# Kernel optimization log

Hardware: AMD Instinct MI355X
Metric: run time of the kernel (lower is better)

## Reference

```python
import jax, jax.numpy as jnp
import numpy as np

HIDDEN = 32
ODE_H = 0.1      # rk4 fixed step size (torchdiffeq options step_size=0.1)
ODE_STEPS = 10   # integrate t in [0, 1]


def gcn_conv(x, W, b, edge_index, n):
    """PyG GCNConv: symmetric norm with self-loops; x' = D^-1/2 (A+I) D^-1/2 (x W) + b."""
    h = x @ W                                  # [n, out]
    src, dst = edge_index[0], edge_index[1]
    deg = jnp.ones((n,), h.dtype).at[dst].add(1.0)   # +1 for self-loop
    dinv = jax.lax.rsqrt(deg)
    coef = (dinv[src] * dinv[dst])[:, None]
    agg = jnp.zeros_like(h).at[dst].add(h[src] * coef)
    agg = agg + h * (dinv * dinv)[:, None]     # self-loop term
    return agg + b


def ode_rk4(x0, edge_index, Wg, bg, wt, n):
    """RK4 integration of psi(t,x)=relu(GCN(x)) * sigmoid(t * wt) from t=0 to 1."""
    def f(t, x):
        gate = jax.nn.sigmoid(t * wt)          # [hidden], Linear(1,h,no bias).sigmoid()
        return jax.nn.relu(gcn_conv(x, Wg, bg, edge_index, n)) * gate

    h = ODE_H
    def step(x, t):
        k1 = f(t, x)
        k2 = f(t + h * 0.5, x + (h * 0.5) * k1)
        k3 = f(t + h * 0.5, x + (h * 0.5) * k2)
        k4 = f(t + h, x + h * k3)
        return x + (h / 6.0) * (k1 + 2.0 * k2 + 2.0 * k3 + k4), None

    ts = jnp.arange(ODE_STEPS, dtype=x0.dtype) * h
    xf, _ = jax.lax.scan(step, x0, ts)
    return xf


def setup_inputs() -> dict:
    key = jax.random.key(0)
    ks = jax.random.split(key, 16)
    N, IN, H = 100000, 128, HIDDEN
    E, DE = 1600000, 800000

    inp = {
        "H_t": jax.random.normal(ks[0], (N, IN), jnp.float32),
        "A_pos_t": jax.random.randint(ks[1], (2, E), 0, N),
        "A_neg_t": jax.random.randint(ks[2], (2, E), 0, N),
        "dA_pos": jax.random.randint(ks[3], (2, DE), 0, N),
        "dA_neg": jax.random.randint(ks[4], (2, DE), 0, N),
        # init GCN
        "W_init": jax.random.normal(ks[5], (IN, H), jnp.float32) / np.sqrt(IN),
        "b_init": jnp.zeros((H,), jnp.float32),
        # pos ODE func
        "W_pos": jax.random.normal(ks[6], (H, H), jnp.float32) / np.sqrt(H),
        "b_pos": jnp.zeros((H,), jnp.float32),
        "wt_pos": jax.random.normal(ks[7], (H,), jnp.float32),
        # neg ODE func
        "W_neg": jax.random.normal(ks[8], (H, H), jnp.float32) / np.sqrt(H),
        "b_neg": jnp.zeros((H,), jnp.float32),
        "wt_neg": jax.random.normal(ks[9], (H,), jnp.float32),
        # combine + layernorm
        "W_comb": jax.random.normal(ks[10], (2 * H, H), jnp.float32) / np.sqrt(2 * H),
        "b_comb": jnp.zeros((H,), jnp.float32),
        "ln_g": jnp.ones((H,), jnp.float32),
        "ln_b": jnp.zeros((H,), jnp.float32),
    }
    return inp


def reference(H_t, A_pos_t, A_neg_t, dA_pos, dA_neg,
              W_init, b_init, W_pos, b_pos, wt_pos,
              W_neg, b_neg, wt_neg, W_comb, b_comb, ln_g, ln_b):
    n = H_t.shape[0]
    edges_all = jnp.concatenate([A_pos_t, A_neg_t], axis=1)
    H = jax.nn.relu(gcn_conv(H_t, W_init, b_init, edges_all, n))   # [n, hidden]
    Z_pos = ode_rk4(H, dA_pos, W_pos, b_pos, wt_pos, n)
    Z_neg = ode_rk4(H, dA_neg, W_neg, b_neg, wt_neg, n)
    Z = jnp.concatenate([Z_pos, Z_neg], axis=-1) @ W_comb + b_comb # [n, hidden]
    mu = jnp.mean(Z, axis=-1, keepdims=True)
    var = jnp.var(Z, axis=-1, keepdims=True)
    return (Z - mu) * jax.lax.rsqrt(var + 1e-5) * ln_g + ln_b
```

## Files before the change

### kernel.cpp

```cpp
#include <hip/hip_runtime.h>
#include <math.h>


#define TPB 256
#define SCAN_T 1024

typedef _Float16 h8 __attribute__((ext_vector_type(8)));
typedef float f8 __attribute__((ext_vector_type(8)));


struct SegG { const int* src; const int* dst; int n; int goff; };
struct FSeg { const int* src; const int* dst; int n; const int* offs; int* cur; };

__global__ __launch_bounds__(TPB) void count_mm(
        SegG s0, SegG s1, SegG s2, SegG s3, int* __restrict__ cnt3,
        unsigned short* __restrict__ rank,
        const float* __restrict__ x, const float* __restrict__ W,
        float* __restrict__ temp, int N, int cntB, int mmB) {
    __shared__ float Ws[128][32];
    __shared__ float xs[8][128];

    int g5 = blockIdx.x / 5, r5 = blockIdx.x % 5;
    if (r5 < 3) {
        int cb = g5 * 3 + r5;
        if (cb >= cntB) return;
        int i = cb * TPB + threadIdx.x;
        SegG s; int e;
        if (i < s0.n) { s = s0; e = i; }
        else if (i < s0.n + s1.n) { s = s1; e = i - s0.n; }
        else if (i < s0.n + s1.n + s2.n) { s = s2; e = i - s0.n - s1.n; }
        else if (i < s0.n + s1.n + s2.n + s3.n) { s = s3; e = i - s0.n - s1.n - s2.n; }
        else return;
        int r = atomicAdd(&cnt3[s.goff + s.dst[e]], 1);
        if (rank) rank[i] = (unsigned short)r;
    } else {
        int mb = g5 * 2 + (r5 - 3);
        if (mb >= mmB) return;
        int tid = threadIdx.x;
        for (int i = tid; i < 128 * 32; i += TPB) Ws[i >> 5][i & 31] = W[i];
        int base = mb * 8;
        for (int i = tid; i < 8 * 128; i += TPB) {
            int idx = base * 128 + i;
            xs[i >> 7][i & 127] = (idx < N * 128) ? x[idx] : 0.0f;
        }
        __syncthreads();
        int row = tid >> 5, c = tid & 31;
        int gr = base + row;
        float acc = 0.0f;
#pragma unroll
        for (int k = 0; k < 128; ++k) acc += xs[row][k] * Ws[k][c];
        if (gr < N) temp[gr * 32 + c] = acc;
    }
}

__global__ __launch_bounds__(TPB) void fill_scale(
        SegG s0, SegG s1, SegG s2, SegG s3,
        const int* __restrict__ offs3, const unsigned short* __restrict__ rank,
        int* __restrict__ csr,
        const float* __restrict__ temp, const float* __restrict__ dinv,
        _Float16* __restrict__ hs, int N, int fillB, int scaleB) {
    int g13 = blockIdx.x / 13, r13 = blockIdx.x % 13;
    if (r13 < 12) {
        int fb = g13 * 12 + r13;
        if (fb >= fillB) return;
        int i = fb * TPB + threadIdx.x;
        SegG s; int e;
        if (i < s0.n) { s = s0; e = i; }
        else if (i < s0.n + s1.n) { s = s1; e = i - s0.n; }
        else if (i < s0.n + s1.n + s2.n) { s = s2; e = i - s0.n - s1.n; }
        else if (i < s0.n + s1.n + s2.n + s3.n) { s = s3; e = i - s0.n - s1.n - s2.n; }
        else return;
        csr[offs3[s.goff + s.dst[e]] + (int)rank[i]] = s.src[e];
    } else {
        int c = g13 * TPB + threadIdx.x;
        if (c < N * 4) {
            f8 v = ((const f8*)temp)[c];
            float dv = dinv[c >> 2];
            ((h8*)hs)[c] = __builtin_convertvector(v * dv, h8);
        }
    }
}

__global__ void scale_hs(const float* __restrict__ temp, const float* __restrict__ dinv,
                         _Float16* __restrict__ hs, int N) {
    int c = blockIdx.x * blockDim.x + threadIdx.x;
    if (c < N * 4) {
        f8 v = ((const f8*)temp)[c];
        ((h8*)hs)[c] = __builtin_convertvector(v * dinv[c >> 2], h8);
    }
}

__global__ void fill4(FSeg s0, FSeg s1, FSeg s2, FSeg s3, int* __restrict__ csr) {
    int i = blockIdx.x * blockDim.x + threadIdx.x;
    FSeg s; int e;
    if (i < s0.n) { s = s0; e = i; }
    else if (i < s0.n + s1.n) { s = s1; e = i - s0.n; }
    else if (i < s0.n + s1.n + s2.n) { s = s2; e = i - s0.n - s1.n; }
    else if (i < s0.n + s1.n + s2.n + s3.n) { s = s3; e = i - s0.n - s1.n - s2.n; }
    else return;
    int d = s.dst[e];
    int pos = s.offs[d] + atomicAdd(&s.cur[d], 1);
    csr[pos] = s.src[e];
}

__global__ void scan_block(const int* __restrict__ in, int n, int* __restrict__ out,
                           int* __restrict__ bsums, float* __restrict__ dinv) {
    __shared__ int sh[SCAN_T];
    int tx = threadIdx.x;
    int g = blockIdx.x * SCAN_T + tx;
    int v = (g < n) ? in[g] : 0;
    if (g < n) dinv[g] = rsqrtf(1.0f + (float)v);
    sh[tx] = v;
    __syncthreads();
    for (int off = 1; off < SCAN_T; off <<= 1) {
        int t = (tx >= off) ? sh[tx - off] : 0;
        __syncthreads();
        sh[tx] += t;
        __syncthreads();
    }
    if (g < n) out[g] = sh[tx] - v;
    if (tx == SCAN_T - 1) bsums[blockIdx.x] = sh[tx];
}

__global__ void scan_sums(int* __restrict__ bsums, int nb) {
    __shared__ int sh[SCAN_T];
    int tx = threadIdx.x;
    int v = (tx < nb) ? bsums[tx] : 0;
    sh[tx] = v;
    __syncthreads();
    for (int off = 1; off < SCAN_T; off <<= 1) {
        int t = (tx >= off) ? sh[tx - off] : 0;
        __syncthreads();
        sh[tx] += t;
        __syncthreads();
    }
    if (tx < nb) bsums[tx] = sh[tx] - v;
}

__global__ void scan_add(int* __restrict__ offs, const int* __restrict__ bsums, int n, int total) {
    int g = blockIdx.x * blockDim.x + threadIdx.x;
    if (g < n) offs[g] += bsums[g >> 10];
    if (g == 0) offs[n] = total;
}

__global__ void scan_add2(int* __restrict__ offs, const int* __restrict__ bsums,
                          int n, int total, int nbs) {
    __shared__ int sb[SCAN_T];
    int tid = threadIdx.x;
    for (int i = tid; i < nbs; i += TPB) sb[i] = bsums[i];
    __syncthreads();
    int g = blockIdx.x * TPB + tid;
    if (g < n) {
        int b = g >> 10;
        int pre = 0;
        for (int j = 0; j < b; ++j) pre += sb[j];
        offs[g] += pre;
    }
    if (g == 0) offs[n] = total;
}


__global__ void mm32_kernel(const float* __restrict__ x, const float* __restrict__ W,
                            const float* __restrict__ dinv, _Float16* __restrict__ hs, int N) {
    __shared__ float Ws[32][32];
    __shared__ float xs[8][32];
    int tid = threadIdx.x;
    for (int i = tid; i < 32 * 32; i += TPB) Ws[i >> 5][i & 31] = W[i];
    int base = blockIdx.x * 8;
    {
        int idx = base * 32 + tid;
        xs[tid >> 5][tid & 31] = (idx < N * 32) ? x[idx] : 0.0f;
    }
    __syncthreads();
    int row = tid >> 5, c = tid & 31;
    int gr = base + row;
    float acc = 0.0f;
#pragma unroll
    for (int k = 0; k < 32; ++k) acc += xs[row][k] * Ws[k][c];
    if (gr < N) hs[gr * 32 + c] = (_Float16)(acc * dinv[gr]);
}


struct Job {
    const int* offs; const int* csr;
    const _Float16* hs_in; _Float16* hs_out;
    const float* dinv; const float* dinv_next;
    const float* bias; const float* wt;
    _Float16* ksum; float* x;
    const float* W;
    const float* W2; const float* dinv2; _Float16* hs_out2;
};

__global__ __launch_bounds__(TPB) void agg_stage(Job jp, Job jn, int nbg, float t,
                                                 int stage, int do_mm, int split,
                                                 float* __restrict__ x2, int N) {
    __shared__ float Ws[32][32];
    __shared__ float Ws2[32][32];
    __shared__ float xts[64][36];
    __shared__ int soffs[65];

    bool isP; int bid;
    if (split) {
        int xcd = blockIdx.x & 7;
        isP = xcd < 4;
        bid = ((int)blockIdx.x >> 3) * 4 + (xcd & 3);
        if (bid >= nbg) return;
    } else {
        isP = (int)blockIdx.x < nbg;
        bid = isP ? blockIdx.x : (blockIdx.x - nbg);
    }
    const Job& J = isP ? jp : jn;
    int nbase = bid * 64;
    int tid = threadIdx.x;
    int lnode = tid >> 2, q = tid & 3;
    int node = nbase + lnode;
    bool valid = node < N;

    if (do_mm) {
        for (int i = tid; i < 32 * 32; i += TPB) Ws[i >> 5][i & 31] = J.W[i];
        if (J.W2) {
            for (int i = tid; i < 32 * 32; i += TPB) Ws2[i >> 5][i & 31] = J.W2[i];
        }
    }
    if (tid < 65) {
        int ix = nbase + tid; if (ix > N) ix = N;
        soffs[tid] = J.offs[ix];
    }
    __syncthreads();

    f8 xrow;
#pragma unroll
    for (int j = 0; j < 8; ++j) xrow[j] = 0.f;

    if (valid) {
        const h8* hsv = (const h8*)J.hs_in;
        const int* __restrict__ csr = J.csr;
        int r0 = soffs[lnode], r1 = soffs[lnode + 1];
        f8 acc = __builtin_convertvector(hsv[node * 4 + q], f8);
        int i = r0;
        for (; i + 4 <= r1; i += 4) {
            int e0 = csr[i], e1 = csr[i + 1], e2 = csr[i + 2], e3 = csr[i + 3];
            h8 v0 = hsv[e0 * 4 + q];
            h8 v1 = hsv[e1 * 4 + q];
            h8 v2 = hsv[e2 * 4 + q];
            h8 v3 = hsv[e3 * 4 + q];
            acc += (__builtin_convertvector(v0, f8) + __builtin_convertvector(v1, f8))
                 + (__builtin_convertvector(v2, f8) + __builtin_convertvector(v3, f8));
        }
        for (; i < r1; ++i)
            acc += __builtin_convertvector(hsv[csr[i] * 4 + q], f8);

        float dv = J.dinv[node];
        f8 bb = ((const f8*)J.bias)[q];
        f8 kv;
#pragma unroll
        for (int j = 0; j < 8; ++j) kv[j] = fmaxf(acc[j] * dv + bb[j], 0.f);
        if (J.wt) {
            f8 w = ((const f8*)J.wt)[q];
#pragma unroll
            for (int j = 0; j < 8; ++j) kv[j] *= 1.f / (1.f + expf(-t * w[j]));
        }
        int idx = node * 4 + q;
        f8* x8 = (f8*)J.x;
        h8* ks8 = (h8*)J.ksum;
        if (stage == 0) {
            x8[idx] = kv;
            ((f8*)x2)[idx] = kv;
            xrow = kv;
        } else if (stage == 4) {
            f8 ks = __builtin_convertvector(ks8[idx], f8);
            f8 xv = x8[idx];
            const float cc = 0.1f / 6.0f;
#pragma unroll
            for (int j = 0; j < 8; ++j) xv[j] += cc * (ks[j] + kv[j]);
            x8[idx] = xv;
            xrow = xv;
        } else {
            float a = (stage == 3) ? 0.1f : 0.05f;
            f8 xv = x8[idx];
#pragma unroll
            for (int j = 0; j < 8; ++j) xrow[j] = xv[j] + a * kv[j];
            if (stage == 1) {
                ks8[idx] = __builtin_convertvector(kv, h8);
            } else {
                f8 ks = __builtin_convertvector(ks8[idx], f8);
#pragma unroll
                for (int j = 0; j < 8; ++j) ks[j] += 2.f * kv[j];
                ks8[idx] = __builtin_convertvector(ks, h8);
            }
        }
    }

    if (do_mm) {
        if (valid) {
#pragma unroll
            for (int j = 0; j < 8; ++j) xts[lnode][q * 8 + j] = xrow[j];
        }
        __syncthreads();
        if (valid) {
            f8 accm;
#pragma unroll
            for (int j = 0; j < 8; ++j) accm[j] = 0.f;
#pragma unroll
            for (int k = 0; k < 32; ++k) {
                float xv = xts[lnode][k];
                f8 w = *(const f8*)&Ws[k][q * 8];
                accm += xv * w;
            }
            accm *= J.dinv_next[node];
            ((h8*)J.hs_out)[node * 4 + q] = __builtin_convertvector(accm, h8);
            if (J.W2) {
                f8 acc2;
#pragma unroll
                for (int j = 0; j < 8; ++j) acc2[j] = 0.f;
#pragma unroll
                for (int k = 0; k < 32; ++k) {
                    float xv = xts[lnode][k];
                    f8 w = *(const f8*)&Ws2[k][q * 8];
                    acc2 += xv * w;
                }
                acc2 *= J.dinv2[node];
                ((h8*)J.hs_out2)[node * 4 + q] = __builtin_convertvector(acc2, h8);
            }
        }
    }
}

__global__ __launch_bounds__(TPB) void stage4_combine(
        Job jp, Job jn, float t,
        const float* __restrict__ Wc, const float* __restrict__ bc,
        const float* __restrict__ lg, const float* __restrict__ lb,
        float* __restrict__ out, int N) {
    __shared__ float Ws[64][32];
    __shared__ float xts[64][68];
    __shared__ int soffs[65];

    int tid = threadIdx.x;
    for (int i = tid; i < 64 * 32; i += TPB) Ws[i >> 5][i & 31] = Wc[i];
    int nbase = blockIdx.x * 64;
    int lnode = tid >> 2, q = tid & 3;
    int node = nbase + lnode;
    bool valid = node < N;

    for (int side = 0; side < 2; ++side) {
        const Job& J = side ? jn : jp;
        __syncthreads();
        if (tid < 65) {
            int ix = nbase + tid; if (ix > N) ix = N;
            soffs[tid] = J.offs[ix];
        }
        __syncthreads();
        if (valid) {
            const h8* hsv = (const h8*)J.hs_in;
            const int* __restrict__ csr = J.csr;
            int r0 = soffs[lnode], r1 = soffs[lnode + 1];
            f8 acc = __builtin_convertvector(hsv[node * 4 + q], f8);
            int i = r0;
            for (; i + 4 <= r1; i += 4) {
                int e0 = csr[i], e1 = csr[i + 1], e2 = csr[i + 2], e3 = csr[i + 3];
                h8 v0 = hsv[e0 * 4 + q];
                h8 v1 = hsv[e1 * 4 + q];
                h8 v2 = hsv[e2 * 4 + q];
                h8 v3 = hsv[e3 * 4 + q];
                acc += (__builtin_convertvector(v0, f8) + __builtin_convertvector(v1, f8))
                     + (__builtin_convertvector(v2, f8) + __builtin_convertvector(v3, f8));
            }
            for (; i < r1; ++i)
                acc += __builtin_convertvector(hsv[csr[i] * 4 + q], f8);

            float dv = J.dinv[node];
            f8 bb = ((const f8*)J.bias)[q];
            f8 kv;
#pragma unroll
            for (int j = 0; j < 8; ++j) kv[j] = fmaxf(acc[j] * dv + bb[j], 0.f);
            f8 w = ((const f8*)J.wt)[q];
#pragma unroll
            for (int j = 0; j < 8; ++j) kv[j] *= 1.f / (1.f + expf(-t * w[j]));

            int idx = node * 4 + q;
            f8 ks = __builtin_convertvector(((const h8*)J.ksum)[idx], f8);
            f8 xv = ((const f8*)J.x)[idx];
            const float cc = 0.1f / 6.0f;
#pragma unroll
            for (int j = 0; j < 8; ++j)
                xts[lnode][side * 32 + q * 8 + j] = xv[j] + cc * (ks[j] + kv[j]);
        }
    }
    __syncthreads();

    if (valid) {
        f8 bcv = ((const f8*)bc)[q];
        f8 accm;
#pragma unroll
        for (int j = 0; j < 8; ++j) accm[j] = bcv[j];
#pragma unroll
        for (int k = 0; k < 64; ++k) {
            float xv = xts[lnode][k];
            f8 w = *(const f8*)&Ws[k][q * 8];
            accm += xv * w;
        }
        float s = 0.f, sq = 0.f;
#pragma unroll
        for (int j = 0; j < 8; ++j) { s += accm[j]; sq += accm[j] * accm[j]; }
        s += __shfl_xor(s, 1); s += __shfl_xor(s, 2);
        sq += __shfl_xor(sq, 1); sq += __shfl_xor(sq, 2);
        float mu = s * (1.0f / 32.0f);
        float var = sq * (1.0f / 32.0f) - mu * mu;
        float rs = rsqrtf(var + 1e-5f);
        f8 gv = ((const f8*)lg)[q];
        f8 bv = ((const f8*)lb)[q];
        f8 o;
#pragma unroll
        for (int j = 0; j < 8; ++j) o[j] = (accm[j] - mu) * rs * gv[j] + bv[j];
        ((f8*)out)[node * 4 + q] = o;
    }
}


__global__ void combine_kernel(const float* __restrict__ zp, const float* __restrict__ zn,
                               const float* __restrict__ Wc, const float* __restrict__ bc,
                               const float* __restrict__ g, const float* __restrict__ be,
                               float* __restrict__ out, int N) {
    __shared__ float Ws[64][32];
    __shared__ float zs[8][64];
    int tid = threadIdx.x;
    for (int i = tid; i < 64 * 32; i += TPB) Ws[i >> 5][i & 31] = Wc[i];
    int base = blockIdx.x * 8;
    {
        int r = tid >> 5, c = tid & 31;
        int gr = base + r;
        zs[r][c] = (gr < N) ? zp[gr * 32 + c] : 0.0f;
        zs[r][32 + c] = (gr < N) ? zn[gr * 32 + c] : 0.0f;
    }
    __syncthreads();
    int row = tid >> 5, c = tid & 31;
    int gr = base + row;
    float acc = bc[c];
#pragma unroll
    for (int k = 0; k < 64; ++k) acc += zs[row][k] * Ws[k][c];
    float s = acc, sq = acc * acc;
#pragma unroll
    for (int off = 16; off; off >>= 1) {
        s += __shfl_xor(s, off, 32);
        sq += __shfl_xor(sq, off, 32);
    }
    float mu = s * (1.0f / 32.0f);
    float var = sq * (1.0f / 32.0f) - mu * mu;
    float y = (acc - mu) * rsqrtf(var + 1e-5f) * g[c] + be[c];
    if (gr < N) out[gr * 32 + c] = y;
}


extern "C" void kernel_launch(void* const* d_in, const int* in_sizes, int n_in,
                              void* d_out, int out_size, void* d_ws, size_t ws_size,
                              hipStream_t stream) {
    const float* H_t = (const float*)d_in[0];
    const int* Apos = (const int*)d_in[1];
    const int* Aneg = (const int*)d_in[2];
    const int* dApos = (const int*)d_in[3];
    const int* dAneg = (const int*)d_in[4];
    const float* W_init = (const float*)d_in[5];
    const float* b_init = (const float*)d_in[6];
    const float* W_pos = (const float*)d_in[7];
    const float* b_pos = (const float*)d_in[8];
    const float* wt_pos = (const float*)d_in[9];
    const float* W_neg = (const float*)d_in[10];
    const float* b_neg = (const float*)d_in[11];
    const float* wt_neg = (const float*)d_in[12];
    const float* W_comb = (const float*)d_in[13];
    const float* b_comb = (const float*)d_in[14];
    const float* ln_g = (const float*)d_in[15];
    const float* ln_b = (const float*)d_in[16];

    const int N = in_sizes[0] / 128;
    const int E1 = in_sizes[1] / 2;
    const int E2 = in_sizes[2] / 2;
    const int DE1 = in_sizes[3] / 2;
    const int DE2 = in_sizes[4] / 2;
    const int Etot = E1 + E2 + DE1 + DE2;
    const int n3 = 3 * N;

    const int* Apos_src = Apos, * Apos_dst = Apos + E1;
    const int* Aneg_src = Aneg, * Aneg_dst = Aneg + E2;
    const int* dApos_src = dApos, * dApos_dst = dApos + DE1;
    const int* dAneg_src = dAneg, * dAneg_dst = dAneg + DE2;

    const size_t n32 = (size_t)N * 32;
    const size_t szf = n32 * 4;
    const size_t szh = n32 * 2;
    auto al = [](size_t b) { return (b + 255) & ~(size_t)255; };

    size_t small_bytes = 3 * al((size_t)n3 * 4)
                       + al(((size_t)n3 + 1) * 4)
                       + al((size_t)Etot * 4)
                       + al(SCAN_T * 4);
    size_t need_merged = 2 * al(szf) + 6 * al(szh) + small_bytes;
    size_t need_rank = need_merged + al((size_t)Etot * 2);
    bool merged = ws_size >= need_merged + 4096;
    bool use_rank = ws_size >= need_rank + 4096;

    char* p = (char*)d_ws;
    auto alloc = [&](size_t bytes) -> void* {
        void* r = (void*)p;
        p += al(bytes);
        return r;
    };
    float* x_pos = (float*)alloc(szf);
    float* x_neg = (float*)alloc(szf);
    _Float16* ksum_p = (_Float16*)alloc(szh);
    _Float16* ksum_n = merged ? (_Float16*)alloc(szh) : ksum_p;
    _Float16* hs_pa = (_Float16*)alloc(szh);
    _Float16* hs_pb = (_Float16*)alloc(szh);
    _Float16* hs_na = merged ? (_Float16*)alloc(szh) : hs_pa;
    _Float16* hs_nb = merged ? (_Float16*)alloc(szh) : hs_pb;
    float* dinv3 = (float*)alloc((size_t)n3 * 4);
    int* cnt3 = (int*)alloc((size_t)n3 * 4);
    int* cur3 = (int*)alloc((size_t)n3 * 4);
    int* offs3 = (int*)alloc(((size_t)n3 + 1) * 4);
    int* csr3 = (int*)alloc((size_t)Etot * 4);
    int* bsums = (int*)alloc(SCAN_T * 4);
    unsigned short* rank = use_rank ? (unsigned short*)alloc((size_t)Etot * 2) : nullptr;

    hipMemsetAsync(cnt3, 0, 2 * al((size_t)n3 * 4), stream);

    float* dinv_all = dinv3, * dinv_pos = dinv3 + N, * dinv_neg = dinv3 + 2 * N;
    const int* offs_all = offs3, * offs_pos = offs3 + N, * offs_neg = offs3 + 2 * N;

    dim3 blk(TPB);
    auto gblk = [](int n) { return dim3((n + TPB - 1) / TPB); };
    dim3 grid_rows((N + 7) / 8);
    const int nb64 = (N + 63) / 64;
    const int nbs = (n3 + SCAN_T - 1) / SCAN_T;
    const int nsplit = ((nb64 + 3) / 4) * 8;

    SegG s0 = { Apos_src, Apos_dst, E1, 0 };
    SegG s1 = { Aneg_src, Aneg_dst, E2, 0 };
    SegG s2 = { dApos_src, dApos_dst, DE1, N };
    SegG s3 = { dAneg_src, dAneg_dst, DE2, 2 * N };
    const int cntB = (Etot + TPB - 1) / TPB;
    const int mmB = (N + 7) / 8;
    {
        const int g5 = max((cntB + 2) / 3, (mmB + 1) / 2);
        count_mm<<<dim3(5 * g5), blk, 0, stream>>>(s0, s1, s2, s3, cnt3, rank,
                                                   H_t, W_init, x_pos, N, cntB, mmB);
    }
    scan_block<<<nbs, SCAN_T, 0, stream>>>(cnt3, n3, offs3, bsums, dinv3);
    if (nbs <= SCAN_T / 4 * 4 && nbs <= 1024) {
        scan_add2<<<gblk(n3), blk, 0, stream>>>(offs3, bsums, n3, Etot, nbs);
    } else {
        scan_sums<<<1, SCAN_T, 0, stream>>>(bsums, nbs);
        scan_add<<<gblk(n3), blk, 0, stream>>>(offs3, bsums, n3, Etot);
    }
    const int scaleB = (N * 4 + TPB - 1) / TPB;
    if (use_rank) {
        const int g13 = max((cntB + 11) / 12, scaleB);
        fill_scale<<<dim3(13 * g13), blk, 0, stream>>>(s0, s1, s2, s3, offs3, rank, csr3,
                                                       x_pos, dinv_all, hs_pa, N, cntB, scaleB);
    } else {
        scale_hs<<<gblk(N * 4), blk, 0, stream>>>(x_pos, dinv_all, hs_pa, N);
        FSeg f0 = { Apos_src, Apos_dst, E1, offs3, cur3 };
        FSeg f1 = { Aneg_src, Aneg_dst, E2, offs3, cur3 };
        FSeg f2 = { dApos_src, dApos_dst, DE1, offs3 + N, cur3 + N };
        FSeg f3 = { dAneg_src, dAneg_dst, DE2, offs3 + 2 * N, cur3 + 2 * N };
        fill4<<<gblk(Etot), blk, 0, stream>>>(f0, f1, f2, f3, csr3);
    }

    auto mkjob = [&](const int* offs, const _Float16* hs_in, _Float16* hs_out,
                     const float* dinv, const float* dinv_next, const float* bias,
                     const float* wt, _Float16* ksum, float* x, const float* W) {
        Job j; j.offs = offs; j.csr = csr3; j.hs_in = hs_in; j.hs_out = hs_out;
        j.dinv = dinv; j.dinv_next = dinv_next; j.bias = bias; j.wt = wt;
        j.ksum = ksum; j.x = x; j.W = W;
        j.W2 = nullptr; j.dinv2 = nullptr; j.hs_out2 = nullptr; return j;
    };

    {
        Job j0 = mkjob(offs_all, hs_pa, hs_pb, dinv_all, dinv_pos, b_init,
                       nullptr, nullptr, x_pos, W_pos);
        if (merged) { j0.W2 = W_neg; j0.dinv2 = dinv_neg; j0.hs_out2 = hs_nb; }
        agg_stage<<<nb64, blk, 0, stream>>>(j0, j0, nb64, 0.0f, 0, 1, 0, x_neg, N);
    }

    if (merged) {
        for (int s = 0; s < 10; ++s) {
            float t0 = 0.1f * (float)s;
            Job p1 = mkjob(offs_pos, hs_pb, hs_pa, dinv_pos, dinv_pos, b_pos, wt_pos, ksum_p, x_pos, W_pos);
            Job n1 = mkjob(offs_neg, hs_nb, hs_na, dinv_neg, dinv_neg, b_neg, wt_neg, ksum_n, x_neg, W_neg);
            agg_stage<<<nsplit, blk, 0, stream>>>(p1, n1, nb64, t0, 1, 1, 1, nullptr, N);
            Job p2 = p1; p2.hs_in = hs_pa; p2.hs_out = hs_pb;
            Job n2 = n1; n2.hs_in = hs_na; n2.hs_out = hs_nb;
            agg_stage<<<nsplit, blk, 0, stream>>>(p2, n2, nb64, t0 + 0.05f, 2, 1, 1, nullptr, N);
            agg_stage<<<nsplit, blk, 0, stream>>>(p1, n1, nb64, t0 + 0.05f, 3, 1, 1, nullptr, N);
            if (s < 9) {
                agg_stage<<<nsplit, blk, 0, stream>>>(p2, n2, nb64, t0 + 0.1f, 4, 1, 1, nullptr, N);
            } else {
                stage4_combine<<<nb64, blk, 0, stream>>>(p2, n2, t0 + 0.1f,
                                                         W_comb, b_comb, ln_g, ln_b,
                                                         (float*)d_out, N);
            }
        }
    } else {
        for (int ode = 0; ode < 2; ++ode) {
            float* x = ode ? x_neg : x_pos;
            const float* W = ode ? W_neg : W_pos;
            const float* b = ode ? b_neg : b_pos;
            const float* wt = ode ? wt_neg : wt_pos;
            const float* dinv = ode ? dinv_neg : dinv_pos;
            const int* offs = ode ? offs_neg : offs_pos;
            if (ode == 1) {
                mm32_kernel<<<grid_rows, blk, 0, stream>>>(x, W, dinv, hs_pb, N);
            }
            for (int s = 0; s < 10; ++s) {
                float t0 = 0.1f * (float)s;
                int last_mm = (s == 9) ? 0 : 1;
                Job j1 = mkjob(offs, hs_pb, hs_pa, dinv, dinv, b, wt, ksum_p, x, W);
                Job j2 = j1; j2.hs_in = hs_pa; j2.hs_out = hs_pb;
                agg_stage<<<nb64, blk, 0, stream>>>(j1, j1, nb64, t0, 1, 1, 0, nullptr, N);
                agg_stage<<<nb64, blk, 0, stream>>>(j2, j2, nb64, t0 + 0.05f, 2, 1, 0, nullptr, N);
                agg_stage<<<nb64, blk, 0, stream>>>(j1, j1, nb64, t0 + 0.05f, 3, 1, 0, nullptr, N);
                agg_stage<<<nb64, blk, 0, stream>>>(j2, j2, nb64, t0 + 0.1f, 4, last_mm, 0, nullptr, N);
            }
        }
        combine_kernel<<<grid_rows, blk, 0, stream>>>(x_pos, x_neg, W_comb, b_comb, ln_g, ln_b,
                                                      (float*)d_out, N);
    }
}
```

Baseline: 1.954 ms.

## Split CSR build so ODE-graph counting and fill overlap init GCN stages

The CSR build is split into two phases. The init-graph edges are counted and scanned first. Counting the two ODE-graph edge sets is folded into the init fill/scale kernel, and their CSR fill is folded into a new stage0 kernel that runs alongside the initial GCN aggregation. This shortens the serial preprocessing chain so the later-needed edge sets are handled under other work. It also strips the stage-0 and W2 paths out of agg_stage to slim that kernel, at the cost of an extra scan pass and more kernel variants.

```diff
diff --git a/kernel.cpp b/kernel.cpp
--- a/kernel.cpp
+++ b/kernel.cpp
@@ -11,6 +11,45 @@
 
 struct SegG { const int* src; const int* dst; int n; int goff; };
 struct FSeg { const int* src; const int* dst; int n; const int* offs; int* cur; };
+
+__global__ __launch_bounds__(TPB) void count_mm_all(
+        SegG s0, SegG s1, int* __restrict__ cnt3,
+        unsigned short* __restrict__ rank,
+        const float* __restrict__ x, const float* __restrict__ W,
+        float* __restrict__ temp, int N, int cntB, int mmB) {
+    __shared__ float Ws[128][32];
+    __shared__ float xs[8][128];
+
+    int g2 = blockIdx.x >> 1, r2 = blockIdx.x & 1;
+    if (r2 == 0) {
+        int cb = g2;
+        if (cb >= cntB) return;
+        int i = cb * TPB + threadIdx.x;
+        SegG s; int e;
+        if (i < s0.n) { s = s0; e = i; }
+        else if (i < s0.n + s1.n) { s = s1; e = i - s0.n; }
+        else return;
+        int r = atomicAdd(&cnt3[s.dst[e]], 1);
+        if (rank) rank[i] = (unsigned short)r;
+    } else {
+        int mb = g2;
+        if (mb >= mmB) return;
+        int tid = threadIdx.x;
+        for (int i = tid; i < 128 * 32; i += TPB) Ws[i >> 5][i & 31] = W[i];
+        int base = mb * 8;
+        for (int i = tid; i < 8 * 128; i += TPB) {
+            int idx = base * 128 + i;
+            xs[i >> 7][i & 127] = (idx < N * 128) ? x[idx] : 0.0f;
+        }
+        __syncthreads();
+        int row = tid >> 5, c = tid & 31;
+        int gr = base + row;
+        float acc = 0.0f;
+#pragma unroll
+        for (int k = 0; k < 128; ++k) acc += xs[row][k] * Ws[k][c];
+        if (gr < N) temp[gr * 32 + c] = acc;
+    }
+}
 
 __global__ __launch_bounds__(TPB) void count_mm(
         SegG s0, SegG s1, SegG s2, SegG s3, int* __restrict__ cnt3,
@@ -53,31 +92,39 @@
     }
 }
 
-__global__ __launch_bounds__(TPB) void fill_scale(
-        SegG s0, SegG s1, SegG s2, SegG s3,
-        const int* __restrict__ offs3, const unsigned short* __restrict__ rank,
+__global__ __launch_bounds__(TPB) void fill_scale_count(
+        SegG a0, SegG a1, SegG p2, SegG p3,
+        const int* __restrict__ offs3, unsigned short* __restrict__ rank,
         int* __restrict__ csr,
         const float* __restrict__ temp, const float* __restrict__ dinv,
-        _Float16* __restrict__ hs, int N, int fillB, int scaleB) {
-    int g13 = blockIdx.x / 13, r13 = blockIdx.x % 13;
-    if (r13 < 12) {
-        int fb = g13 * 12 + r13;
+        _Float16* __restrict__ hs, int* __restrict__ cnt3,
+        int N, int Eall, int fillB, int scaleB, int cntB) {
+    int g = blockIdx.x / 13, r = blockIdx.x % 13;
+    if (r < 8) {
+        int fb = g * 8 + r;
         if (fb >= fillB) return;
         int i = fb * TPB + threadIdx.x;
         SegG s; int e;
-        if (i < s0.n) { s = s0; e = i; }
-        else if (i < s0.n + s1.n) { s = s1; e = i - s0.n; }
-        else if (i < s0.n + s1.n + s2.n) { s = s2; e = i - s0.n - s1.n; }
-        else if (i < s0.n + s1.n + s2.n + s3.n) { s = s3; e = i - s0.n - s1.n - s2.n; }
+        if (i < a0.n) { s = a0; e = i; }
+        else if (i < a0.n + a1.n) { s = a1; e = i - a0.n; }
         else return;
-        csr[offs3[s.goff + s.dst[e]] + (int)rank[i]] = s.src[e];
-    } else {
-        int c = g13 * TPB + threadIdx.x;
+        csr[offs3[s.dst[e]] + (int)rank[i]] = s.src[e];
+    } else if (r == 8) {
+        int c = g * TPB + threadIdx.x;
         if (c < N * 4) {
             f8 v = ((const f8*)temp)[c];
-            float dv = dinv[c >> 2];
-            ((h8*)hs)[c] = __builtin_convertvector(v * dv, h8);
-        }
+            ((h8*)hs)[c] = __builtin_convertvector(v * dinv[c >> 2], h8);
+        }
+    } else {
+        int cb = g * 4 + (r - 9);
+        if (cb >= cntB) return;
+        int j = cb * TPB + threadIdx.x;
+        SegG s; int e;
+        if (j < p2.n) { s = p2; e = j; }
+        else if (j < p2.n + p3.n) { s = p3; e = j - p2.n; }
+        else return;
+        int rr = atomicAdd(&cnt3[s.goff + s.dst[e]], 1);
+        rank[Eall + j] = (unsigned short)rr;
     }
 }
 
@@ -137,14 +184,15 @@
     if (tx < nb) bsums[tx] = sh[tx] - v;
 }
 
-__global__ void scan_add(int* __restrict__ offs, const int* __restrict__ bsums, int n, int total) {
+__global__ void scan_add(int* __restrict__ offs, const int* __restrict__ bsums, int n,
+                         int total, int base) {
     int g = blockIdx.x * blockDim.x + threadIdx.x;
-    if (g < n) offs[g] += bsums[g >> 10];
-    if (g == 0) offs[n] = total;
+    if (g < n) offs[g] += bsums[g >> 10] + base;
+    if (g == 0) offs[n] = base + total;
 }
 
 __global__ void scan_add2(int* __restrict__ offs, const int* __restrict__ bsums,
-                          int n, int total, int nbs) {
+                          int n, int total, int nbs, int base) {
     __shared__ int sb[SCAN_T];
     int tid = threadIdx.x;
     for (int i = tid; i < nbs; i += TPB) sb[i] = bsums[i];
@@ -154,9 +202,9 @@
         int b = g >> 10;
         int pre = 0;
         for (int j = 0; j < b; ++j) pre += sb[j];
-        offs[g] += pre;
-    }
-    if (g == 0) offs[n] = total;
+        offs[g] += pre + base;
+    }
+    if (g == 0) offs[n] = base + total;
 }
 
 
@@ -191,11 +239,113 @@
     const float* W2; const float* dinv2; _Float16* hs_out2;
 };
 
-__global__ __launch_bounds__(TPB) void agg_stage(Job jp, Job jn, int nbg, float t,
-                                                 int stage, int do_mm, int split,
-                                                 float* __restrict__ x2, int N) {
+__global__ __launch_bounds__(TPB) void stage0_fill(
+        Job J, SegG p2, SegG p3,
+        const int* __restrict__ offs3, const unsigned short* __restrict__ rank,
+        int* __restrict__ csr, int Eall,
+        float* __restrict__ x2, int N, int nbg, int fillB) {
     __shared__ float Ws[32][32];
     __shared__ float Ws2[32][32];
+    __shared__ float xts[64][36];
+    __shared__ int soffs[65];
+
+    int g = blockIdx.x / 5, r = blockIdx.x % 5;
+    if (r != 0) {
+        int fb = g * 4 + (r - 1);
+        if (fb >= fillB) return;
+        int j = fb * TPB + threadIdx.x;
+        SegG s; int e;
+        if (j < p2.n) { s = p2; e = j; }
+        else if (j < p2.n + p3.n) { s = p3; e = j - p2.n; }
+        else return;
+        csr[offs3[s.goff + s.dst[e]] + (int)rank[Eall + j]] = s.src[e];
+        return;
+    }
+    int bid = g;
+    if (bid >= nbg) return;
+
+    int nbase = bid * 64;
+    int tid = threadIdx.x;
+    int lnode = tid >> 2, q = tid & 3;
+    int node = nbase + lnode;
+    bool valid = node < N;
+
+    for (int i = tid; i < 32 * 32; i += TPB) Ws[i >> 5][i & 31] = J.W[i];
+    if (J.W2) {
+        for (int i = tid; i < 32 * 32; i += TPB) Ws2[i >> 5][i & 31] = J.W2[i];
+    }
+    if (tid < 65) {
+        int ix = nbase + tid; if (ix > N) ix = N;
+        soffs[tid] = J.offs[ix];
+    }
+    __syncthreads();
+
+    f8 xrow;
+#pragma unroll
+    for (int j = 0; j < 8; ++j) xrow[j] = 0.f;
+
+    if (valid) {
+        const h8* hsv = (const h8*)J.hs_in;
+        const int* __restrict__ csre = J.csr;
+        int r0 = soffs[lnode], r1 = soffs[lnode + 1];
+        f8 acc = __builtin_convertvector(hsv[node * 4 + q], f8);
+        int i = r0;
+        for (; i + 4 <= r1; i += 4) {
+            int e0 = csre[i], e1 = csre[i + 1], e2 = csre[i + 2], e3 = csre[i + 3];
+            h8 v0 = hsv[e0 * 4 + q];
+            h8 v1 = hsv[e1 * 4 + q];
+            h8 v2 = hsv[e2 * 4 + q];
+            h8 v3 = hsv[e3 * 4 + q];
+            acc += (__builtin_convertvector(v0, f8) + __builtin_convertvector(v1, f8))
+                 + (__builtin_convertvector(v2, f8) + __builtin_convertvector(v3, f8));
+        }
+        for (; i < r1; ++i)
+            acc += __builtin_convertvector(hsv[csre[i] * 4 + q], f8);
+
+        float dv = J.dinv[node];
+        f8 bb = ((const f8*)J.bias)[q];
+        f8 kv;
+#pragma unroll
+        for (int j = 0; j < 8; ++j) kv[j] = fmaxf(acc[j] * dv + bb[j], 0.f);
+        int idx = node * 4 + q;
+        ((f8*)J.x)[idx] = kv;
+        ((f8*)x2)[idx] = kv;
+        xrow = kv;
+#pragma unroll
+        for (int j = 0; j < 8; ++j) xts[lnode][q * 8 + j] = xrow[j];
+    }
+    __syncthreads();
+    if (valid) {
+        f8 accm;
+#pragma unroll
+        for (int j = 0; j < 8; ++j) accm[j] = 0.f;
+#pragma unroll
+        for (int k = 0; k < 32; ++k) {
+            float xv = xts[lnode][k];
+            f8 w = *(const f8*)&Ws[k][q * 8];
+            accm += xv * w;
+        }
+        accm *= J.dinv_next[node];
+        ((h8*)J.hs_out)[node * 4 + q] = __builtin_convertvector(accm, h8);
+        if (J.W2) {
+            f8 acc2;
+#pragma unroll
+            for (int j = 0; j < 8; ++j) acc2[j] = 0.f;
+#pragma unroll
+            for (int k = 0; k < 32; ++k) {
+                float xv = xts[lnode][k];
+                f8 w = *(const f8*)&Ws2[k][q * 8];
+                acc2 += xv * w;
+            }
+            acc2 *= J.dinv2[node];
+            ((h8*)J.hs_out2)[node * 4 + q] = __builtin_convertvector(acc2, h8);
+        }
+    }
+}
+
+__global__ __launch_bounds__(TPB) void agg_stage(Job jp, Job jn, int nbg, float t,
+                                                 int stage, int do_mm, int split, int N) {
+    __shared__ float Ws[32][32];
     __shared__ float xts[64][36];
     __shared__ int soffs[65];
 
@@ -218,9 +368,6 @@
 
     if (do_mm) {
         for (int i = tid; i < 32 * 32; i += TPB) Ws[i >> 5][i & 31] = J.W[i];
-        if (J.W2) {
-            for (int i = tid; i < 32 * 32; i += TPB) Ws2[i >> 5][i & 31] = J.W2[i];
-        }
     }
     if (tid < 65) {
         int ix = nbase + tid; if (ix > N) ix = N;
@@ -255,19 +402,14 @@
         f8 kv;
 #pragma unroll
         for (int j = 0; j < 8; ++j) kv[j] = fmaxf(acc[j] * dv + bb[j], 0.f);
-        if (J.wt) {
-            f8 w = ((const f8*)J.wt)[q];
-#pragma unroll
-            for (int j = 0; j < 8; ++j) kv[j] *= 1.f / (1.f + expf(-t * w[j]));
-        }
+        f8 w = ((const f8*)J.wt)[q];
+#pragma unroll
+        for (int j = 0; j < 8; ++j) kv[j] *= 1.f / (1.f + expf(-t * w[j]));
+
         int idx = node * 4 + q;
         f8* x8 = (f8*)J.x;
         h8* ks8 = (h8*)J.ksum;
-        if (stage == 0) {
-            x8[idx] = kv;
-            ((f8*)x2)[idx] = kv;
-            xrow = kv;
-        } else if (stage == 4) {
+        if (stage == 4) {
             f8 ks = __builtin_convertvector(ks8[idx], f8);
             f8 xv = x8[idx];
             const float cc = 0.1f / 6.0f;
@@ -309,19 +451,6 @@
             }
             accm *= J.dinv_next[node];
             ((h8*)J.hs_out)[node * 4 + q] = __builtin_convertvector(accm, h8);
-            if (J.W2) {
-                f8 acc2;
-#pragma unroll
-                for (int j = 0; j < 8; ++j) acc2[j] = 0.f;
-#pragma unroll
-                for (int k = 0; k < 32; ++k) {
-                    float xv = xts[lnode][k];
-                    f8 w = *(const f8*)&Ws2[k][q * 8];
-                    acc2 += xv * w;
-                }
-                acc2 *= J.dinv2[node];
-                ((h8*)J.hs_out2)[node * 4 + q] = __builtin_convertvector(acc2, h8);
-            }
         }
     }
 }
@@ -477,7 +606,9 @@
     const int E2 = in_sizes[2] / 2;
     const int DE1 = in_sizes[3] / 2;
     const int DE2 = in_sizes[4] / 2;
-    const int Etot = E1 + E2 + DE1 + DE2;
+    const int Eall = E1 + E2;
+    const int Epn = DE1 + DE2;
+    const int Etot = Eall + Epn;
     const int n3 = 3 * N;
 
     const int* Apos_src = Apos, * Apos_dst = Apos + E1;
@@ -530,40 +661,14 @@
     auto gblk = [](int n) { return dim3((n + TPB - 1) / TPB); };
     dim3 grid_rows((N + 7) / 8);
     const int nb64 = (N + 63) / 64;
-    const int nbs = (n3 + SCAN_T - 1) / SCAN_T;
     const int nsplit = ((nb64 + 3) / 4) * 8;
-
-    SegG s0 = { Apos_src, Apos_dst, E1, 0 };
-    SegG s1 = { Aneg_src, Aneg_dst, E2, 0 };
-    SegG s2 = { dApos_src, dApos_dst, DE1, N };
-    SegG s3 = { dAneg_src, dAneg_dst, DE2, 2 * N };
-    const int cntB = (Etot + TPB - 1) / TPB;
     const int mmB = (N + 7) / 8;
-    {
-        const int g5 = max((cntB + 2) / 3, (mmB + 1) / 2);
-        count_mm<<<dim3(5 * g5), blk, 0, stream>>>(s0, s1, s2, s3, cnt3, rank,
-                                                   H_t, W_init, x_pos, N, cntB, mmB);
-    }
-    scan_block<<<nbs, SCAN_T, 0, stream>>>(cnt3, n3, offs3, bsums, dinv3);
-    if (nbs <= SCAN_T / 4 * 4 && nbs <= 1024) {
-        scan_add2<<<gblk(n3), blk, 0, stream>>>(offs3, bsums, n3, Etot, nbs);
-    } else {
-        scan_sums<<<1, SCAN_T, 0, stream>>>(bsums, nbs);
-        scan_add<<<gblk(n3), blk, 0, stream>>>(offs3, bsums, n3, Etot);
-    }
     const int scaleB = (N * 4 + TPB - 1) / TPB;
-    if (use_rank) {
-        const int g13 = max((cntB + 11) / 12, scaleB);
-        fill_scale<<<dim3(13 * g13), blk, 0, stream>>>(s0, s1, s2, s3, offs3, rank, csr3,
-                                                       x_pos, dinv_all, hs_pa, N, cntB, scaleB);
-    } else {
-        scale_hs<<<gblk(N * 4), blk, 0, stream>>>(x_pos, dinv_all, hs_pa, N);
-        FSeg f0 = { Apos_src, Apos_dst, E1, offs3, cur3 };
-        FSeg f1 = { Aneg_src, Aneg_dst, E2, offs3, cur3 };
-        FSeg f2 = { dApos_src, dApos_dst, DE1, offs3 + N, cur3 + N };
-        FSeg f3 = { dAneg_src, dAneg_dst, DE2, offs3 + 2 * N, cur3 + 2 * N };
-        fill4<<<gblk(Etot), blk, 0, stream>>>(f0, f1, f2, f3, csr3);
-    }
+
+    SegG a0 = { Apos_src, Apos_dst, E1, 0 };
+    SegG a1 = { Aneg_src, Aneg_dst, E2, 0 };
+    SegG p2 = { dApos_src, dApos_dst, DE1, N };
+    SegG p3 = { dAneg_src, dAneg_dst, DE2, 2 * N };
 
     auto mkjob = [&](const int* offs, const _Float16* hs_in, _Float16* hs_out,
                      const float* dinv, const float* dinv_next, const float* bias,
@@ -574,27 +679,75 @@
         j.W2 = nullptr; j.dinv2 = nullptr; j.hs_out2 = nullptr; return j;
     };
 
-    {
-        Job j0 = mkjob(offs_all, hs_pa, hs_pb, dinv_all, dinv_pos, b_init,
-                       nullptr, nullptr, x_pos, W_pos);
-        if (merged) { j0.W2 = W_neg; j0.dinv2 = dinv_neg; j0.hs_out2 = hs_nb; }
-        agg_stage<<<nb64, blk, 0, stream>>>(j0, j0, nb64, 0.0f, 0, 1, 0, x_neg, N);
+    if (use_rank) {
+        const int cntBall = (Eall + TPB - 1) / TPB;
+        count_mm_all<<<dim3(2 * max(cntBall, mmB)), blk, 0, stream>>>(
+            a0, a1, cnt3, rank, H_t, W_init, x_pos, N, cntBall, mmB);
+        const int nbsA = (N + SCAN_T - 1) / SCAN_T;
+        scan_block<<<nbsA, SCAN_T, 0, stream>>>(cnt3, N, offs3, bsums, dinv3);
+        scan_add2<<<gblk(N), blk, 0, stream>>>(offs3, bsums, N, Eall, nbsA, 0);
+        const int cntBpn = (Epn + TPB - 1) / TPB;
+        {
+            const int g13 = max(max((cntBall + 7) / 8, scaleB), (cntBpn + 3) / 4);
+            fill_scale_count<<<dim3(13 * g13), blk, 0, stream>>>(
+                a0, a1, p2, p3, offs3, rank, csr3, x_pos, dinv_all, hs_pa,
+                cnt3, N, Eall, cntBall, scaleB, cntBpn);
+        }
+        const int nbsP = (2 * N + SCAN_T - 1) / SCAN_T;
+        scan_block<<<nbsP, SCAN_T, 0, stream>>>(cnt3 + N, 2 * N, offs3 + N, bsums, dinv3 + N);
+        scan_add2<<<gblk(2 * N), blk, 0, stream>>>(offs3 + N, bsums, 2 * N, Epn, nbsP, Eall);
+        {
+            Job j0 = mkjob(offs_all, hs_pa, hs_pb, dinv_all, dinv_pos, b_init,
+                           nullptr, nullptr, x_pos, W_pos);
+            if (merged) { j0.W2 = W_neg; j0.dinv2 = dinv_neg; j0.hs_out2 = hs_nb; }
+            const int g5 = max(nb64, (cntBpn + 3) / 4);
+            stage0_fill<<<dim3(5 * g5), blk, 0, stream>>>(
+                j0, p2, p3, offs3, rank, csr3, Eall, x_neg, N, nb64, cntBpn);
+        }
+    } else {
+        const int cntB = (Etot + TPB - 1) / TPB;
+        {
+            const int g5 = max((cntB + 2) / 3, (mmB + 1) / 2);
+            count_mm<<<dim3(5 * g5), blk, 0, stream>>>(a0, a1, p2, p3, cnt3, nullptr,
+                                                       H_t, W_init, x_pos, N, cntB, mmB);
+        }
+        const int nbs = (n3 + SCAN_T - 1) / SCAN_T;
+        scan_block<<<nbs, SCAN_T, 0, stream>>>(cnt3, n3, offs3, bsums, dinv3);
+        if (nbs <= 1024) {
+            scan_add2<<<gblk(n3), blk, 0, stream>>>(offs3, bsums, n3, Etot, nbs, 0);
+        } else {
+            scan_sums<<<1, SCAN_T, 0, stream>>>(bsums, nbs);
+            scan_add<<<gblk(n3), blk, 0, stream>>>(offs3, bsums, n3, Etot, 0);
+        }
+        scale_hs<<<gblk(N * 4), blk, 0, stream>>>(x_pos, dinv_all, hs_pa, N);
+        FSeg f0 = { Apos_src, Apos_dst, E1, offs3, cur3 };
+        FSeg f1 = { Aneg_src, Aneg_dst, E2, offs3, cur3 };
+        FSeg f2 = { dApos_src, dApos_dst, DE1, offs3 + N, cur3 + N };
+        FSeg f3 = { dAneg_src, dAneg_dst, DE2, offs3 + 2 * N, cur3 + 2 * N };
+        fill4<<<gblk(Etot), blk, 0, stream>>>(f0, f1, f2, f3, csr3);
+        {
+            Job j0 = mkjob(offs_all, hs_pa, hs_pb, dinv_all, dinv_pos, b_init,
+                           nullptr, nullptr, x_pos, W_pos);
+            if (merged) { j0.W2 = W_neg; j0.dinv2 = dinv_neg; j0.hs_out2 = hs_nb; }
+            stage0_fill<<<dim3(5 * nb64), blk, 0, stream>>>(
+                j0, p2, p3, offs3, rank, csr3, Eall, x_neg, N, nb64, 0);
+        }
     }
 
     if (merged) {
         for (int s = 0; s < 10; ++s) {
             float t0 = 0.1f * (float)s;
-            Job p1 = mkjob(offs_pos, hs_pb, hs_pa, dinv_pos, dinv_pos, b_pos, wt_pos, ksum_p, x_pos, W_pos);
-            Job n1 = mkjob(offs_neg, hs_nb, hs_na, dinv_neg, dinv_neg, b_neg, wt_neg, ksum_n, x_neg, W_neg);
-            agg_stage<<<nsplit, blk, 0, stream>>>(p1, n1, nb64, t0, 1, 1, 1, nullptr, N);
-            Job p2 = p1; p2.hs_in = hs_pa; p2.hs_out = hs_pb;
-            Job n2 = n1; n2.hs_in = hs_na; n2.hs_out = hs_nb;
-            agg_stage<<<nsplit, blk, 0, stream>>>(p2, n2, nb64, t0 + 0.05f, 2, 1, 1, nullptr, N);
-            agg_stage<<<nsplit, blk, 0, stream>>>(p1, n1, nb64, t0 + 0.05f, 3, 1, 1, nullptr, N);
+            Job p1j = mkjob(offs_pos, hs_pb, hs_pa, dinv_pos, dinv_pos, b_pos, wt_pos, ksum_p, x_pos, W_pos);
+            Job n1j = mkjob(offs_neg, hs_nb, hs_na, dinv_neg, dinv_neg, b_neg, wt_neg, ksum_n, x_neg, W_neg);
+            agg_stage<<<nsplit, blk, 0, stream>>>(p1j, n1j, nb64, t0, 1, 1, 1, N);
+            Job p2j = p1j; p2j.hs_in = hs_pa; p2j.hs_out = hs_pb;
+            Job n2j = n1j; n2j.hs_in = hs_na; n2j.hs_out = hs_nb;
+            agg_stage<<<nsplit, blk, 0, stream>>>(p2j, n2j, nb64, t0 + 0.05f, 2, 1, 1, N);
+            agg_stage<<<nsplit, blk, 0, stream>>>(p1j, n1j, nb64, t0 + 0.05f, 3, 1, 1, N);
             if (s < 9) {
-                agg_stage<<<nsplit, blk, 0, stream>>>(p2, n2, nb64, t0 + 0.1f, 4, 1, 1, nullptr, N);
+                agg_stage<<<nsplit, blk, 0, stream>>>(p2j, n2j, nb64, t0 + 0.1f, 4, 1, 1, N);
             } else {
-                stage4_combine<<<nb64, blk, 0, stream>>>(p2, n2, t0 + 0.1f,
+                stage4_combine<<<nb64, blk, 0, stream>>>(p2j, n2j, t0 + 0.1f,
                                                          W_comb, b_comb, ln_g, ln_b,
                                                          (float*)d_out, N);
             }
@@ -615,10 +768,10 @@
                 int last_mm = (s == 9) ? 0 : 1;
                 Job j1 = mkjob(offs, hs_pb, hs_pa, dinv, dinv, b, wt, ksum_p, x, W);
                 Job j2 = j1; j2.hs_in = hs_pa; j2.hs_out = hs_pb;
-                agg_stage<<<nb64, blk, 0, stream>>>(j1, j1, nb64, t0, 1, 1, 0, nullptr, N);
-                agg_stage<<<nb64, blk, 0, stream>>>(j2, j2, nb64, t0 + 0.05f, 2, 1, 0, nullptr, N);
-                agg_stage<<<nb64, blk, 0, stream>>>(j1, j1, nb64, t0 + 0.05f, 3, 1, 0, nullptr, N);
-                agg_stage<<<nb64, blk, 0, stream>>>(j2, j2, nb64, t0 + 0.1f, 4, last_mm, 0, nullptr, N);
+                agg_stage<<<nb64, blk, 0, stream>>>(j1, j1, nb64, t0, 1, 1, 0, N);
+                agg_stage<<<nb64, blk, 0, stream>>>(j2, j2, nb64, t0 + 0.05f, 2, 1, 0, N);
+                agg_stage<<<nb64, blk, 0, stream>>>(j1, j1, nb64, t0 + 0.05f, 3, 1, 0, N);
+                agg_stage<<<nb64, blk, 0, stream>>>(j2, j2, nb64, t0 + 0.1f, 4, last_mm, 0, N);
             }
         }
         combine_kernel<<<grid_rows, blk, 0, stream>>>(x_pos, x_neg, W_comb, b_comb, ln_g, ln_b,
```

Measured after the change: 1.908 ms. -2.4%, faster.
